# Kernel optimization log

Hardware: AMD Instinct MI355X
Metric: run time of the kernel (lower is better)

## Reference

```python
import jax, jax.numpy as jnp
import numpy as np

B, N, F, T = 32, 2048, 16, 64


def setup_inputs() -> dict:
    key = jax.random.key(0)
    ks = jax.random.split(key, 6)
    return {
        "x": jax.random.normal(ks[0], (B, N, F, T), dtype=jnp.float32),
        "U1": jax.random.normal(ks[1], (N, 1), dtype=jnp.float32) * (1.0 / np.sqrt(N)),
        "U2": jax.random.normal(ks[2], (F, N), dtype=jnp.float32) * (1.0 / np.sqrt(F)),
        "U3": jax.random.normal(ks[3], (1, F), dtype=jnp.float32) * (1.0 / np.sqrt(F)),
        "be": jax.random.normal(ks[4], (1, T, T), dtype=jnp.float32),
        "Ve": jax.random.normal(ks[5], (T, T), dtype=jnp.float32) * (1.0 / np.sqrt(T)),
    }


def reference(x, U1, U2, U3, be, Ve):
    # x: (B, N, F, T)
    # lhs = squeeze(x^T(0,3,2,1) @ U1) @ U2 : contract N then project F->N -> (B, T, N)
    lhs = jnp.einsum("bnft,n->btf", x, U1[:, 0]) @ U2  # (B, T, N)
    # rhs = squeeze(U3 @ x, -2): contract F -> (B, N, T)
    rhs = jnp.einsum("f,bnft->bnt", U3[0], x)  # (B, N, T)
    product = jnp.matmul(lhs, rhs)  # (B, T, T)
    E = jnp.einsum("ts,bsu->btu", Ve, jax.nn.sigmoid(product + be))  # (B, T, T)
    return jax.nn.softmax(E, axis=1)
```

## Files before the change

### kernel.cpp

```cpp
#include <hip/hip_runtime.h>
#include <hip/hip_bf16.h>
#include <math.h>


#define B_ 32
#define N_ 2048
#define F_ 16
#define T_ 64
#define NPB 64
#define CHUNKS (N_ / NPB)

__global__ __launch_bounds__(256, 6) void ta_pass1(
    const float* __restrict__ x, const float* __restrict__ U1,
    const float* __restrict__ U2, const float* __restrict__ U3,
    float* __restrict__ partial)
{
  const int blk    = blockIdx.x;
  const int b      = blk / CHUNKS;
  const int chunk  = blk % CHUNKS;
  const int n_base = chunk * NPB;
  const int tid    = threadIdx.x;
  const int lane   = tid & 63;
  const int w      = tid >> 6;
  const int g      = lane >> 4;
  const int tq     = lane & 15;

  __shared__ float4 u2q[NPB][4];
  __shared__ float4 zred[4][256];

  for (int i = tid; i < NPB * F_; i += 256) {
    const int f = i >> 6, n = i & 63;
    reinterpret_cast<float*>(&u2q[n][f & 3])[f >> 2] = U2[f * N_ + n_base + n];
  }
  const float u3own = U3[tid >> 4];
  __syncthreads();

  float4 ya  = make_float4(0.f, 0.f, 0.f, 0.f);
  float4 za0 = ya, za1 = ya, za2 = ya, za3 = ya;

  const float4* xb = reinterpret_cast<const float4*>(x)
                   + ((size_t)b * N_ + n_base) * 256;
  #pragma unroll 4
  for (int n = 0; n < NPB; ++n) {
    const float4 v  = xb[n * 256 + tid];
    const float  u1 = U1[n_base + n];
    ya.x = fmaf(u1, v.x, ya.x);
    ya.y = fmaf(u1, v.y, ya.y);
    ya.z = fmaf(u1, v.z, ya.z);
    ya.w = fmaf(u1, v.w, ya.w);
    float4 rp;
    rp.x = u3own * v.x; rp.y = u3own * v.y;
    rp.z = u3own * v.z; rp.w = u3own * v.w;
    rp.x += __shfl_xor(rp.x, 16); rp.y += __shfl_xor(rp.y, 16);
    rp.z += __shfl_xor(rp.z, 16); rp.w += __shfl_xor(rp.w, 16);
    rp.x += __shfl_xor(rp.x, 32); rp.y += __shfl_xor(rp.y, 32);
    rp.z += __shfl_xor(rp.z, 32); rp.w += __shfl_xor(rp.w, 32);
    const float4 u2v = u2q[n][g];
    za0.x = fmaf(u2v.x, rp.x, za0.x); za0.y = fmaf(u2v.x, rp.y, za0.y);
    za0.z = fmaf(u2v.x, rp.z, za0.z); za0.w = fmaf(u2v.x, rp.w, za0.w);
    za1.x = fmaf(u2v.y, rp.x, za1.x); za1.y = fmaf(u2v.y, rp.y, za1.y);
    za1.z = fmaf(u2v.y, rp.z, za1.z); za1.w = fmaf(u2v.y, rp.w, za1.w);
    za2.x = fmaf(u2v.z, rp.x, za2.x); za2.y = fmaf(u2v.z, rp.y, za2.y);
    za2.z = fmaf(u2v.z, rp.z, za2.z); za2.w = fmaf(u2v.z, rp.w, za2.w);
    za3.x = fmaf(u2v.w, rp.x, za3.x); za3.y = fmaf(u2v.w, rp.y, za3.y);
    za3.z = fmaf(u2v.w, rp.z, za3.z); za3.w = fmaf(u2v.w, rp.w, za3.w);
  }

  zred[w][(g +  0) * 16 + tq] = za0;
  zred[w][(g +  4) * 16 + tq] = za1;
  zred[w][(g +  8) * 16 + tq] = za2;
  zred[w][(g + 12) * 16 + tq] = za3;
  __syncthreads();

  float4* pb = reinterpret_cast<float4*>(partial + (size_t)blk * 2048);
  pb[tid] = ya;
  const float4 a0 = zred[0][tid], a1 = zred[1][tid];
  const float4 a2 = zred[2][tid], a3 = zred[3][tid];
  float4 zv;
  zv.x = a0.x + a1.x + a2.x + a3.x;
  zv.y = a0.y + a1.y + a2.y + a3.y;
  zv.z = a0.z + a1.z + a2.z + a3.z;
  zv.w = a0.w + a1.w + a2.w + a3.w;
  pb[256 + tid] = zv;
}

__global__ __launch_bounds__(256) void ta_finish(
    const float* __restrict__ partial, const float* __restrict__ be,
    const float* __restrict__ Ve, float* __restrict__ out)
{
  const int b   = blockIdx.x;
  const int tid = threadIdx.x;
  __shared__ float ys[T_][F_ + 1];
  __shared__ float zs[F_][T_];
  __shared__ float sig[T_][T_ + 1];
  __shared__ float Es[T_][T_ + 1];

  const float4* p4 = reinterpret_cast<const float4*>(partial) + (size_t)b * CHUNKS * 512;
  #pragma unroll
  for (int k = 0; k < 2; ++k) {
    const int i4 = tid + k * 256;
    float4 s = make_float4(0.f, 0.f, 0.f, 0.f);
    #pragma unroll 4
    for (int j = 0; j < CHUNKS; ++j) {
      const float4 v = p4[(size_t)j * 512 + i4];
      s.x += v.x; s.y += v.y; s.z += v.z; s.w += v.w;
    }
    if (i4 < 256) {
      const int f = i4 >> 4, t0 = (i4 & 15) * 4;
      ys[t0 + 0][f] = s.x; ys[t0 + 1][f] = s.y;
      ys[t0 + 2][f] = s.z; ys[t0 + 3][f] = s.w;
    } else {
      const int j4 = i4 - 256;
      const int f = j4 >> 4, u0 = (j4 & 15) * 4;
      zs[f][u0 + 0] = s.x; zs[f][u0 + 1] = s.y;
      zs[f][u0 + 2] = s.z; zs[f][u0 + 3] = s.w;
    }
  }
  __syncthreads();

  const int tr = tid >> 2;
  const int ub = (tid & 3) * 16;
  #pragma unroll
  for (int i = 0; i < 16; ++i) {
    const int u = ub + i;
    float acc = 0.f;
    #pragma unroll
    for (int f = 0; f < F_; ++f) acc = fmaf(ys[tr][f], zs[f][u], acc);
    acc += be[tr * T_ + u];
    sig[tr][u] = 1.f / (1.f + __expf(-acc));
  }
  __syncthreads();
  #pragma unroll
  for (int i = 0; i < 16; ++i) {
    const int u = ub + i;
    float acc = 0.f;
    #pragma unroll
    for (int s = 0; s < T_; ++s) acc = fmaf(Ve[tr * T_ + s], sig[s][u], acc);
    Es[tr][u] = acc;
  }
  __syncthreads();

  const int u = tid >> 2, p = tid & 3;
  float m = -INFINITY;
  #pragma unroll
  for (int r = 0; r < 16; ++r) m = fmaxf(m, Es[p * 16 + r][u]);
  m = fmaxf(m, __shfl_xor(m, 1));
  m = fmaxf(m, __shfl_xor(m, 2));
  float den = 0.f;
  #pragma unroll
  for (int r = 0; r < 16; ++r) den += __expf(Es[p * 16 + r][u] - m);
  den += __shfl_xor(den, 1);
  den += __shfl_xor(den, 2);
  const float inv = 1.f / den;
  #pragma unroll
  for (int r = 0; r < 16; ++r)
    out[(size_t)b * T_ * T_ + (p * 16 + r) * T_ + u] =
        __expf(Es[p * 16 + r][u] - m) * inv;
}

extern "C" void kernel_launch(void* const* d_in, const int* in_sizes, int n_in,
                              void* d_out, int out_size, void* d_ws, size_t ws_size,
                              hipStream_t stream) {
  const float* x  = (const float*)d_in[0];
  const float* U1 = (const float*)d_in[1];
  const float* U2 = (const float*)d_in[2];
  const float* U3 = (const float*)d_in[3];
  const float* be = (const float*)d_in[4];
  const float* Ve = (const float*)d_in[5];
  float* out = (float*)d_out;
  float* partial = (float*)d_ws;

  ta_pass1<<<B_ * CHUNKS, 256, 0, stream>>>(x, U1, U2, U3, partial);
  ta_finish<<<B_, 256, 0, stream>>>(partial, be, Ve, out);
}
```

Before: 79.45 us.

## Stage x tiles through LDS with async global_load_lds triple buffering

Pass 1 now copies x into a 3-slot LDS ring with global_load_lds, keeping two tiles in flight ahead of the compute loop, and waits on vmcnt before a barrier at each tile. The chunk size is halved to 32 nodes, so the grid doubles, and the occupancy hint drops to 3 blocks per CU to fit the larger shared memory. The aim is to hide global memory latency in this bandwidth-bound reduction. In exchange there are more per-tile barriers, more partial rows for the finish kernel to sum (its unroll is raised to 8), and a dependence on the exact waitcnt counts being correct.

```diff
diff --git a/kernel.cpp b/kernel.cpp
--- a/kernel.cpp
+++ b/kernel.cpp
@@ -7,17 +7,20 @@
 #define N_ 2048
 #define F_ 16
 #define T_ 64
-#define NPB 64
+#define NPB 32
 #define CHUNKS (N_ / NPB)
-
-__global__ __launch_bounds__(256, 6) void ta_pass1(
+#define TR 4
+#define NT (NPB / TR)
+#define SLOTS 3
+
+__global__ __launch_bounds__(256, 3) void ta_pass1(
     const float* __restrict__ x, const float* __restrict__ U1,
     const float* __restrict__ U2, const float* __restrict__ U3,
     float* __restrict__ partial)
 {
   const int blk    = blockIdx.x;
-  const int b      = blk / CHUNKS;
-  const int chunk  = blk % CHUNKS;
+  const int b      = blk >> 6;
+  const int chunk  = blk & 63;
   const int n_base = chunk * NPB;
   const int tid    = threadIdx.x;
   const int lane   = tid & 63;
@@ -25,57 +28,93 @@
   const int g      = lane >> 4;
   const int tq     = lane & 15;
 
+  __shared__ float4 slots[SLOTS * 1024];
   __shared__ float4 u2q[NPB][4];
-  __shared__ float4 zred[4][256];
-
-  for (int i = tid; i < NPB * F_; i += 256) {
-    const int f = i >> 6, n = i & 63;
-    reinterpret_cast<float*>(&u2q[n][f & 3])[f >> 2] = U2[f * N_ + n_base + n];
-  }
+  __shared__ float  u1s[NPB];
+
   const float u3own = U3[tid >> 4];
-  __syncthreads();
+  const int f0 = tid >> 5, n0 = tid & 31;
+  const int f1 = (tid + 256) >> 5;
+  const float u2a = U2[f0 * N_ + n_base + n0];
+  const float u2b = U2[f1 * N_ + n_base + n0];
+  float u1v = 0.f;
+  if (tid < NPB) u1v = U1[n_base + tid];
+
+  reinterpret_cast<float*>(&u2q[n0][f0 & 3])[f0 >> 2] = u2a;
+  reinterpret_cast<float*>(&u2q[n0][f1 & 3])[f1 >> 2] = u2b;
+  if (tid < NPB) u1s[tid] = u1v;
+
+  const char* xb = reinterpret_cast<const char*>(x)
+                 + ((size_t)b * N_ + n_base) * 4096;
+
+  auto stage_tile = [&](int t) {
+    const char* gsrc = xb + (size_t)t * 16384 + w * 4096 + lane * 16;
+    char* ldst = reinterpret_cast<char*>(slots)
+               + (t % SLOTS) * 16384 + w * 4096;
+    #pragma unroll
+    for (int i = 0; i < 4; ++i) {
+      __builtin_amdgcn_global_load_lds(
+          (const __attribute__((address_space(1))) void*)(gsrc + i * 1024),
+          (__attribute__((address_space(3))) void*)(ldst + i * 1024),
+          16, 0, 0);
+    }
+  };
+
+  stage_tile(0);
+  stage_tile(1);
+  asm volatile("s_waitcnt lgkmcnt(0)" ::: "memory");
+  __builtin_amdgcn_s_barrier();
 
   float4 ya  = make_float4(0.f, 0.f, 0.f, 0.f);
   float4 za0 = ya, za1 = ya, za2 = ya, za3 = ya;
 
-  const float4* xb = reinterpret_cast<const float4*>(x)
-                   + ((size_t)b * N_ + n_base) * 256;
-  #pragma unroll 4
-  for (int n = 0; n < NPB; ++n) {
-    const float4 v  = xb[n * 256 + tid];
-    const float  u1 = U1[n_base + n];
-    ya.x = fmaf(u1, v.x, ya.x);
-    ya.y = fmaf(u1, v.y, ya.y);
-    ya.z = fmaf(u1, v.z, ya.z);
-    ya.w = fmaf(u1, v.w, ya.w);
-    float4 rp;
-    rp.x = u3own * v.x; rp.y = u3own * v.y;
-    rp.z = u3own * v.z; rp.w = u3own * v.w;
-    rp.x += __shfl_xor(rp.x, 16); rp.y += __shfl_xor(rp.y, 16);
-    rp.z += __shfl_xor(rp.z, 16); rp.w += __shfl_xor(rp.w, 16);
-    rp.x += __shfl_xor(rp.x, 32); rp.y += __shfl_xor(rp.y, 32);
-    rp.z += __shfl_xor(rp.z, 32); rp.w += __shfl_xor(rp.w, 32);
-    const float4 u2v = u2q[n][g];
-    za0.x = fmaf(u2v.x, rp.x, za0.x); za0.y = fmaf(u2v.x, rp.y, za0.y);
-    za0.z = fmaf(u2v.x, rp.z, za0.z); za0.w = fmaf(u2v.x, rp.w, za0.w);
-    za1.x = fmaf(u2v.y, rp.x, za1.x); za1.y = fmaf(u2v.y, rp.y, za1.y);
-    za1.z = fmaf(u2v.y, rp.z, za1.z); za1.w = fmaf(u2v.y, rp.w, za1.w);
-    za2.x = fmaf(u2v.z, rp.x, za2.x); za2.y = fmaf(u2v.z, rp.y, za2.y);
-    za2.z = fmaf(u2v.z, rp.z, za2.z); za2.w = fmaf(u2v.z, rp.w, za2.w);
-    za3.x = fmaf(u2v.w, rp.x, za3.x); za3.y = fmaf(u2v.w, rp.y, za3.y);
-    za3.z = fmaf(u2v.w, rp.z, za3.z); za3.w = fmaf(u2v.w, rp.w, za3.w);
-  }
-
-  zred[w][(g +  0) * 16 + tq] = za0;
-  zred[w][(g +  4) * 16 + tq] = za1;
-  zred[w][(g +  8) * 16 + tq] = za2;
-  zred[w][(g + 12) * 16 + tq] = za3;
+  for (int t = 0; t < NT; ++t) {
+    if (t == NT - 1) { asm volatile("s_waitcnt vmcnt(0)" ::: "memory"); }
+    else             { asm volatile("s_waitcnt vmcnt(4)" ::: "memory"); }
+    __builtin_amdgcn_s_barrier();
+    if (t + 2 < NT) stage_tile(t + 2);
+
+    const float4* sl = slots + (t % SLOTS) * 1024;
+    #pragma unroll
+    for (int n = 0; n < TR; ++n) {
+      const float4 v  = sl[n * 256 + tid];
+      const float  u1 = u1s[t * TR + n];
+      ya.x = fmaf(u1, v.x, ya.x);
+      ya.y = fmaf(u1, v.y, ya.y);
+      ya.z = fmaf(u1, v.z, ya.z);
+      ya.w = fmaf(u1, v.w, ya.w);
+      float4 rp;
+      rp.x = u3own * v.x; rp.y = u3own * v.y;
+      rp.z = u3own * v.z; rp.w = u3own * v.w;
+      rp.x += __shfl_xor(rp.x, 16); rp.y += __shfl_xor(rp.y, 16);
+      rp.z += __shfl_xor(rp.z, 16); rp.w += __shfl_xor(rp.w, 16);
+      rp.x += __shfl_xor(rp.x, 32); rp.y += __shfl_xor(rp.y, 32);
+      rp.z += __shfl_xor(rp.z, 32); rp.w += __shfl_xor(rp.w, 32);
+      const float4 u2v = u2q[t * TR + n][g];
+      za0.x = fmaf(u2v.x, rp.x, za0.x); za0.y = fmaf(u2v.x, rp.y, za0.y);
+      za0.z = fmaf(u2v.x, rp.z, za0.z); za0.w = fmaf(u2v.x, rp.w, za0.w);
+      za1.x = fmaf(u2v.y, rp.x, za1.x); za1.y = fmaf(u2v.y, rp.y, za1.y);
+      za1.z = fmaf(u2v.y, rp.z, za1.z); za1.w = fmaf(u2v.y, rp.w, za1.w);
+      za2.x = fmaf(u2v.z, rp.x, za2.x); za2.y = fmaf(u2v.z, rp.y, za2.y);
+      za2.z = fmaf(u2v.z, rp.z, za2.z); za2.w = fmaf(u2v.z, rp.w, za2.w);
+      za3.x = fmaf(u2v.w, rp.x, za3.x); za3.y = fmaf(u2v.w, rp.y, za3.y);
+      za3.z = fmaf(u2v.w, rp.z, za3.z); za3.w = fmaf(u2v.w, rp.w, za3.w);
+    }
+    asm volatile("s_waitcnt lgkmcnt(0)" ::: "memory");
+  }
+
+  __syncthreads();
+  float4* zred = slots;
+  zred[w * 256 + (g +  0) * 16 + tq] = za0;
+  zred[w * 256 + (g +  4) * 16 + tq] = za1;
+  zred[w * 256 + (g +  8) * 16 + tq] = za2;
+  zred[w * 256 + (g + 12) * 16 + tq] = za3;
   __syncthreads();
 
   float4* pb = reinterpret_cast<float4*>(partial + (size_t)blk * 2048);
   pb[tid] = ya;
-  const float4 a0 = zred[0][tid], a1 = zred[1][tid];
-  const float4 a2 = zred[2][tid], a3 = zred[3][tid];
+  const float4 a0 = zred[0 * 256 + tid], a1 = zred[1 * 256 + tid];
+  const float4 a2 = zred[2 * 256 + tid], a3 = zred[3 * 256 + tid];
   float4 zv;
   zv.x = a0.x + a1.x + a2.x + a3.x;
   zv.y = a0.y + a1.y + a2.y + a3.y;
@@ -100,7 +139,7 @@
   for (int k = 0; k < 2; ++k) {
     const int i4 = tid + k * 256;
     float4 s = make_float4(0.f, 0.f, 0.f, 0.f);
-    #pragma unroll 4
+    #pragma unroll 8
     for (int j = 0; j < CHUNKS; ++j) {
       const float4 v = p4[(size_t)j * 512 + i4];
       s.x += v.x; s.y += v.y; s.z += v.z; s.w += v.w;
```

After: 86.50 us. 8.9% more time.

## Fuse reduction and finish kernels via last-block atomic counter, double chunk size

Applied to the files above, without the earlier changes.

Merges the two kernels into one: each block writes its partial sums, bumps a per-batch atomic counter, and the last block for each batch does the cross-chunk reduction and the sigmoid/matmul/softmax epilogue. The chunk size per block goes from 64 to 128 rows, which halves the block count and the partial traffic, and the loops are unrolled further. This removes a second kernel launch and its dependency gap, but adds a memset of the counters, threadfences, and a serialized tail on the last block of each batch. Occupancy hints drop to two blocks per SM, and shared memory grows to a unified buffer.

```diff
diff --git a/kernel.cpp b/kernel.cpp
--- a/kernel.cpp
+++ b/kernel.cpp
@@ -7,17 +7,27 @@
 #define N_ 2048
 #define F_ 16
 #define T_ 64
-#define NPB 64
+#define NPB 128
 #define CHUNKS (N_ / NPB)
+#define PARTIAL_FLOATS ((size_t)B_ * CHUNKS * 2048)
 
-__global__ __launch_bounds__(256, 6) void ta_pass1(
+typedef float f32x4 __attribute__((ext_vector_type(4)));
+
+#define SMEM_BYTES 41728
+
+__global__ __launch_bounds__(256, 2) void ta_fused(
     const float* __restrict__ x, const float* __restrict__ U1,
     const float* __restrict__ U2, const float* __restrict__ U3,
-    float* __restrict__ partial)
+    const float* __restrict__ be, const float* __restrict__ Ve,
+    float* __restrict__ partial, int* __restrict__ counters,
+    float* __restrict__ out)
 {
+  __shared__ __align__(16) char smem[SMEM_BYTES];
+  __shared__ int is_last;
+
   const int blk    = blockIdx.x;
-  const int b      = blk / CHUNKS;
-  const int chunk  = blk % CHUNKS;
+  const int b      = blk >> 4;
+  const int chunk  = blk & 15;
   const int n_base = chunk * NPB;
   const int tid    = threadIdx.x;
   const int lane   = tid & 63;
@@ -25,11 +35,11 @@
   const int g      = lane >> 4;
   const int tq     = lane & 15;
 
-  __shared__ float4 u2q[NPB][4];
-  __shared__ float4 zred[4][256];
+  float4 (*u2q)[4]    = reinterpret_cast<float4(*)[4]>(smem);
+  float4 (*zred)[256] = reinterpret_cast<float4(*)[256]>(smem + 8192);
 
   for (int i = tid; i < NPB * F_; i += 256) {
-    const int f = i >> 6, n = i & 63;
+    const int f = i >> 7, n = i & (NPB - 1);
     reinterpret_cast<float*>(&u2q[n][f & 3])[f >> 2] = U2[f * N_ + n_base + n];
   }
   const float u3own = U3[tid >> 4];
@@ -40,7 +50,7 @@
 
   const float4* xb = reinterpret_cast<const float4*>(x)
                    + ((size_t)b * N_ + n_base) * 256;
-  #pragma unroll 4
+  #pragma unroll 8
   for (int n = 0; n < NPB; ++n) {
     const float4 v  = xb[n * 256 + tid];
     const float  u1 = U1[n_base + n];
@@ -82,25 +92,28 @@
   zv.z = a0.z + a1.z + a2.z + a3.z;
   zv.w = a0.w + a1.w + a2.w + a3.w;
   pb[256 + tid] = zv;
-}
 
-__global__ __launch_bounds__(256) void ta_finish(
-    const float* __restrict__ partial, const float* __restrict__ be,
-    const float* __restrict__ Ve, float* __restrict__ out)
-{
-  const int b   = blockIdx.x;
-  const int tid = threadIdx.x;
-  __shared__ float ys[T_][F_ + 1];
-  __shared__ float zs[F_][T_];
-  __shared__ float sig[T_][T_ + 1];
-  __shared__ float Es[T_][T_ + 1];
+  __threadfence();
+  if (tid == 0) {
+    const int old = atomicAdd(&counters[b], 1);
+    is_last = (old == CHUNKS - 1);
+  }
+  __syncthreads();
+  if (!is_last) return;
+  __threadfence();
 
-  const float4* p4 = reinterpret_cast<const float4*>(partial) + (size_t)b * CHUNKS * 512;
+  float (*ys)[F_ + 1] = reinterpret_cast<float(*)[F_ + 1]>(smem);
+  float (*zs)[T_]     = reinterpret_cast<float(*)[T_]>(smem + 4352);
+  float (*sig)[T_ + 1]= reinterpret_cast<float(*)[T_ + 1]>(smem + 8448);
+  float (*Es)[T_ + 1] = reinterpret_cast<float(*)[T_ + 1]>(smem + 25088);
+
+  const float4* p4 = reinterpret_cast<const float4*>(partial)
+                   + (size_t)b * CHUNKS * 512;
   #pragma unroll
   for (int k = 0; k < 2; ++k) {
     const int i4 = tid + k * 256;
     float4 s = make_float4(0.f, 0.f, 0.f, 0.f);
-    #pragma unroll 4
+    #pragma unroll 8
     for (int j = 0; j < CHUNKS; ++j) {
       const float4 v = p4[(size_t)j * 512 + i4];
       s.x += v.x; s.y += v.y; s.z += v.z; s.w += v.w;
@@ -167,9 +180,11 @@
   const float* U3 = (const float*)d_in[3];
   const float* be = (const float*)d_in[4];
   const float* Ve = (const float*)d_in[5];
-  float* out = (float*)d_out;
-  float* partial = (float*)d_ws;
+  float* out      = (float*)d_out;
+  float* partial  = (float*)d_ws;
+  int*   counters = (int*)((char*)d_ws + PARTIAL_FLOATS * sizeof(float));
 
-  ta_pass1<<<B_ * CHUNKS, 256, 0, stream>>>(x, U1, U2, U3, partial);
-  ta_finish<<<B_, 256, 0, stream>>>(partial, be, Ve, out);
+  hipMemsetAsync(counters, 0, B_ * sizeof(int), stream);
+  ta_fused<<<B_ * CHUNKS, 256, 0, stream>>>(x, U1, U2, U3, be, Ve,
+                                            partial, counters, out);
 }
```

New measurement: 162.5 us. 2.05x slower.
